# Kernel tuning notes

Hardware: AMD Instinct MI355X
Metric: run time of the kernel (lower is better)

Reference implementation:

```python
import jax, jax.numpy as jnp
import numpy as np

B, S, D_IN = 2, 2048, 1024
DIM, H, G = 64, 16, 4  # head dim, num_heads, kv groups


def setup_inputs() -> dict:
    key = jax.random.key(0)
    ks = jax.random.split(key, 9)
    query = jax.random.normal(ks[0], (B, S, D_IN), dtype=jnp.float32)
    key_t = jax.random.normal(ks[1], (B, S, D_IN), dtype=jnp.float32)
    value = jax.random.normal(ks[2], (B, S, D_IN), dtype=jnp.float32)
    # causal mask; masked_fill where mask == 0
    mask = jnp.tril(jnp.ones((S, S), dtype=jnp.int32))[None]  # [1,S,S]
    sc = 1.0 / np.sqrt(D_IN)
    Wq = jax.random.normal(ks[3], (H, D_IN, DIM), dtype=jnp.float32) * sc
    bq = jnp.zeros((H, DIM), dtype=jnp.float32)
    Wk = jax.random.normal(ks[4], (G, D_IN, DIM), dtype=jnp.float32) * sc
    bk = jnp.zeros((G, DIM), dtype=jnp.float32)
    Wv = jax.random.normal(ks[5], (G, D_IN, DIM), dtype=jnp.float32) * sc
    bv = jnp.zeros((G, DIM), dtype=jnp.float32)
    return {"query": query, "key": key_t, "value": value, "mask": mask,
            "Wq": Wq, "bq": bq, "Wk": Wk, "bk": bk, "Wv": Wv, "bv": bv}


def reference(query, key, value, mask, Wq, bq, Wk, bk, Wv, bv):
    # batched per-head projections (replaces the Python loop over heads)
    Q = jnp.einsum('bsd,hde->bhse', query, Wq) + bq[None, :, None, :]   # [B,H,S,E]
    K = jnp.einsum('bsd,gde->bgse', key, Wk) + bk[None, :, None, :]     # [B,G,S,E]
    V = jnp.einsum('bsd,gde->bgse', value, Wv) + bv[None, :, None, :]   # [B,G,S,E]
    # head i uses KV group i % G (as in the original loop)
    g_idx = jnp.arange(H) % G
    Kh = K[:, g_idx]  # [B,H,S,E]
    Vh = V[:, g_idx]
    attn = jnp.einsum('bhqe,bhke->bhqk', Q, Kh) / np.sqrt(DIM)          # [B,H,S,S]
    attn = jnp.where(mask[:, None] == 0, jnp.float32(-1e9), attn)
    p = jax.nn.softmax(attn, axis=-1)
    z = jnp.einsum('bhqk,bhke->bhqe', p, Vh)                             # [B,H,S,E]
    # concat heads along last dim (same order as torch.cat of z_list)
    return z.transpose(0, 2, 1, 3).reshape(B, S, H * DIM)
```

## Files before the change

kernel.cpp:

```cpp
#include <hip/hip_runtime.h>
#include <hip/hip_bf16.h>
#include <math.h>

#define S_LEN 2048
#define DIN   1024
#define NH    16
#define NG    4

typedef short s16x8 __attribute__((ext_vector_type(8)));
typedef float f32x4 __attribute__((ext_vector_type(4)));

__device__ __forceinline__ unsigned short f2bf(float x) {
  union { float f; unsigned u; } v; v.f = x;
  unsigned r = v.u + 0x7FFFu + ((v.u >> 16) & 1u);
  return (unsigned short)(r >> 16);
}
__device__ __forceinline__ unsigned cvtpk(float a, float b) {
  unsigned r;
  asm("v_cvt_pk_bf16_f32 %0, %1, %2" : "=v"(r) : "v"(a), "v"(b));
  return r;
}

#define GLOAD_LDS16(gsrc, ldst)                                              \
  __builtin_amdgcn_global_load_lds(                                         \
      (const __attribute__((address_space(1))) unsigned int*)(gsrc),        \
      (__attribute__((address_space(3))) unsigned int*)(ldst), 16, 0, 0)


__global__ __launch_bounds__(256) void k_cast(
    const float* __restrict__ q, const float* __restrict__ k,
    const float* __restrict__ v, unsigned short* __restrict__ AF) {
  const float* src = (blockIdx.y == 0) ? q : (blockIdx.y == 1) ? k : v;
  unsigned short* dst = AF + (size_t)blockIdx.y * 4194304;
  int flat = blockIdx.x * 256 + threadIdx.x;
  int b = flat >> 18, s = (flat >> 7) & 2047, d0 = (flat & 127) * 8;
  const float* sp = src + (size_t)(b * 2048 + s) * 1024 + d0;
  float4 x = *(const float4*)sp;
  float4 y = *(const float4*)(sp + 4);
  union { s16x8 v; unsigned u[4]; } r;
  r.u[0] = cvtpk(x.x, x.y); r.u[1] = cvtpk(x.z, x.w);
  r.u[2] = cvtpk(y.x, y.y); r.u[3] = cvtpk(y.z, y.w);
  unsigned short* p = dst + (size_t)((b * 128 + (s >> 4)) * 32 + (d0 >> 5)) * 512
                    + (s & 15) * 8 + ((d0 >> 3) & 3) * 128;
  *(s16x8*)p = r.v;
}

__global__ __launch_bounds__(256) void k_wtrans(
    const float* __restrict__ Wq, const float* __restrict__ Wk,
    const float* __restrict__ Wv, unsigned short* __restrict__ WF) {
  __shared__ __align__(16) unsigned short T[64][72];
  const int u = blockIdx.x >> 4, D0 = (blockIdx.x & 15) * 64;
  const int t = threadIdx.x;
  const float* src = (u < 16) ? (Wq + (size_t)u * 65536)
                   : (u < 20) ? (Wk + (size_t)(u - 16) * 65536)
                              : (Wv + (size_t)(u - 20) * 65536);
  const int e4 = (t & 15) * 4, dl = t >> 4;
  #pragma unroll
  for (int p = 0; p < 4; ++p) {
    const int d = p * 16 + dl;
    float4 v = *(const float4*)(src + (size_t)(D0 + d) * 64 + e4);
    T[e4 + 0][d] = f2bf(v.x); T[e4 + 1][d] = f2bf(v.y);
    T[e4 + 2][d] = f2bf(v.z); T[e4 + 3][d] = f2bf(v.w);
  }
  __syncthreads();
  const int j = t & 7;
  #pragma unroll
  for (int p = 0; p < 2; ++p) {
    const int e = p * 32 + (t >> 3);
    unsigned short* dst = WF + (size_t)u * 65536
        + (size_t)((e >> 4) * 32 + (D0 >> 5) + (j >> 2)) * 512
        + (e & 15) * 8 + (j & 3) * 128;
    *(s16x8*)dst = *(const s16x8*)&T[e][j * 8];
  }
}

__global__ __launch_bounds__(256, 4) void k_project(
    const unsigned short* __restrict__ AF,
    const float* __restrict__ bq, const float* __restrict__ bk,
    const float* __restrict__ bv,
    const unsigned short* __restrict__ WF,
    unsigned short* __restrict__ QF,
    unsigned short* __restrict__ KF,
    unsigned short* __restrict__ VF) {
  const int i = blockIdx.x;
  const int lid = (i & 7) * 96 + (i >> 3);
  const int strip = lid / 48;
  const int rr = lid % 48;
  const int b = rr / 24, u = rr % 24;
  const int tid = threadIdx.x;
  const int w = tid >> 6, lane = tid & 63, lq = lane & 15, gq = lane >> 4;

  const unsigned short* AFp = AF
      + (size_t)((u < 16) ? 0 : (u < 20) ? 1 : 2) * 4194304
      + (size_t)b * 2097152;
  const float* bias = (u < 16) ? bq + u * 64
                    : (u < 20) ? bk + (u - 16) * 64 : bv + (u - 20) * 64;
  const unsigned short* WFp = WF + (size_t)u * 65536;
  const int sb0 = strip * 8 + w * 2;
  const float OSC = (u < 16) ? 0.1803368801111204f : 1.0f;

  f32x4 acc[2][4] = {};
  s16x8 aE[2], bE[4], aO[2], bO[4];

  auto LD = [&](s16x8 (&a)[2], s16x8 (&bf)[4], int dk) {
    a[0] = *(const s16x8*)(AFp + (size_t)((sb0 + 0) * 32 + dk) * 512 + lane * 8);
    a[1] = *(const s16x8*)(AFp + (size_t)((sb0 + 1) * 32 + dk) * 512 + lane * 8);
    #pragma unroll
    for (int n = 0; n < 4; ++n)
      bf[n] = *(const s16x8*)(WFp + (size_t)(n * 32 + dk) * 512 + lane * 8);
  };
  auto FM = [&](const s16x8 (&a)[2], const s16x8 (&bf)[4]) {
    #pragma unroll
    for (int rf = 0; rf < 2; ++rf)
      #pragma unroll
      for (int n = 0; n < 4; ++n)
        acc[rf][n] = __builtin_amdgcn_mfma_f32_16x16x32_bf16(a[rf], bf[n], acc[rf][n], 0, 0, 0);
  };

  LD(aE, bE, 0);
  for (int dk = 0; dk < 32; dk += 2) {
    LD(aO, bO, dk + 1);
    FM(aE, bE);
    if (dk + 2 < 32) LD(aE, bE, dk + 2);
    FM(aO, bO);
  }

  float bvv[4];
  #pragma unroll
  for (int n = 0; n < 4; ++n) bvv[n] = bias[n * 16 + lq];

  unsigned short* dst = (u < 16) ? QF + (size_t)(b * 16 + u) * 131072
                      : (u < 20) ? KF + (size_t)(b * 4 + (u - 16)) * 131072
                                 : VF + (size_t)(b * 4 + (u - 20)) * 131072;
  #pragma unroll
  for (int rf = 0; rf < 2; ++rf)
    #pragma unroll
    for (int n = 0; n < 4; ++n)
      #pragma unroll
      for (int r = 0; r < 4; ++r) {
        const int s = strip * 128 + w * 32 + rf * 16 + gq * 4 + r;
        const int d = n * 16 + lq;
        const unsigned short hv = f2bf((acc[rf][n][r] + bvv[n]) * OSC);
        if (u < 20)
          dst[(size_t)((s >> 4) * 2 + (d >> 5)) * 512
              + (s & 15) * 8 + ((d >> 3) & 3) * 128 + (d & 7)] = hv;
        else
          dst[(size_t)(n * 64 + (s >> 5)) * 512
              + lq * 8 + ((s >> 3) & 3) * 128 + (s & 7)] = hv;
      }
}

__global__ __launch_bounds__(256) void k_attn(
    const unsigned short* __restrict__ QF, const unsigned short* __restrict__ KF,
    const unsigned short* __restrict__ VF, float* __restrict__ out) {
  __shared__ __align__(16) unsigned short KV[2][8192];
  __shared__ __align__(16) unsigned short P[4][16][72];
  const int tid = threadIdx.x;
  const int w = tid >> 6, lane = tid & 63, lq = lane & 15, gq = lane >> 4;
  const int x = blockIdx.x;
  const int xcd = x & 7, li = x >> 3;
  const int g = xcd & 3;
  const int j = 127 - (li * 2 + (xcd >> 2));
  const int h = g + 4 * w;
  const int b = blockIdx.y;

  const unsigned short* QFp = QF + (size_t)(b * NH + h) * 131072;
  const unsigned short* KFp = KF + (size_t)(b * NG + g) * 131072;
  const unsigned short* VFp = VF + (size_t)(b * NG + g) * 131072;
  const int nt = (j >> 2) + 1;

  const s16x8 qf0 = *(const s16x8*)(QFp + (size_t)(j * 2 + 0) * 512 + lane * 8);
  const s16x8 qf1 = *(const s16x8*)(QFp + (size_t)(j * 2 + 1) * 512 + lane * 8);
  f32x4 z[4] = {};
  float lsum = 0.f;

  auto stage = [&](int t, int buf) {
    const unsigned short* ks = KFp + (size_t)t * 4096 + (w * 2) * 512 + lane * 8;
    unsigned short* kd = &KV[buf][(w * 2) * 512];
    GLOAD_LDS16(ks, kd);
    GLOAD_LDS16(ks + 512, kd + 512);
    const unsigned short* vs = VFp + (size_t)(w * 64 + t * 2) * 512 + lane * 8;
    unsigned short* vd = &KV[buf][4096 + (w * 2) * 512];
    GLOAD_LDS16(vs, vd);
    GLOAD_LDS16(vs + 512, vd + 512);
  };

  auto tile = [&](int t, int buf) {
    const unsigned short* kb = &KV[buf][0];
    const unsigned short* vb = &KV[buf][4096];
    f32x4 sv[4];
    __builtin_amdgcn_s_setprio(1);
    #pragma unroll
    for (int f = 0; f < 4; ++f) {
      const s16x8 kA = *(const s16x8*)(kb + (f * 2 + 0) * 512 + lane * 8);
      const s16x8 kB = *(const s16x8*)(kb + (f * 2 + 1) * 512 + lane * 8);
      f32x4 s = {};
      s = __builtin_amdgcn_mfma_f32_16x16x32_bf16(kA, qf0, s, 0, 0, 0);
      s = __builtin_amdgcn_mfma_f32_16x16x32_bf16(kB, qf1, s, 0, 0, 0);
      sv[f] = s;
    }
    __builtin_amdgcn_s_setprio(0);
    if (t == nt - 1) {
      const int k0 = t * 64;
      const int qrow = j * 16 + lq;
      #pragma unroll
      for (int f = 0; f < 4; ++f)
        #pragma unroll
        for (int r = 0; r < 4; ++r)
          if (k0 + f * 16 + gq * 4 + r > qrow) sv[f][r] = -1e30f;
    }
    float s0 = 0.f, s1 = 0.f;
    #pragma unroll
    for (int f = 0; f < 4; ++f) {
      float p0 = __builtin_amdgcn_exp2f(sv[f][0]);
      float p1 = __builtin_amdgcn_exp2f(sv[f][1]);
      float p2 = __builtin_amdgcn_exp2f(sv[f][2]);
      float p3 = __builtin_amdgcn_exp2f(sv[f][3]);
      s0 += p0 + p1; s1 += p2 + p3;
      *(uint2*)&P[w][lq][f * 16 + gq * 4] = make_uint2(cvtpk(p0, p1), cvtpk(p2, p3));
    }
    lsum += s0 + s1;
    const s16x8 pa0 = *(const s16x8*)&P[w][lq][gq * 8];
    const s16x8 pa1 = *(const s16x8*)&P[w][lq][32 + gq * 8];
    __builtin_amdgcn_s_setprio(1);
    #pragma unroll
    for (int n = 0; n < 4; ++n) {
      const s16x8 v0 = *(const s16x8*)(vb + (n * 2 + 0) * 512 + lane * 8);
      const s16x8 v1 = *(const s16x8*)(vb + (n * 2 + 1) * 512 + lane * 8);
      z[n] = __builtin_amdgcn_mfma_f32_16x16x32_bf16(pa0, v0, z[n], 0, 0, 0);
      z[n] = __builtin_amdgcn_mfma_f32_16x16x32_bf16(pa1, v1, z[n], 0, 0, 0);
    }
    __builtin_amdgcn_s_setprio(0);
  };

  stage(0, 0);
  asm volatile("s_waitcnt vmcnt(0)");
  __syncthreads();
  int buf = 0;
  for (int t = 0; t < nt; ++t) {
    if (t + 1 < nt) stage(t + 1, buf ^ 1);
    tile(t, buf);
    asm volatile("s_waitcnt vmcnt(0)");
    __syncthreads();
    buf ^= 1;
  }

  lsum += __shfl_xor(lsum, 16);
  lsum += __shfl_xor(lsum, 32);
  float* outp = out + (size_t)b * S_LEN * 1024 + h * 64;
  #pragma unroll
  for (int r = 0; r < 4; ++r) {
    float lr = __shfl(lsum, gq * 4 + r, 64);
    float inv = __builtin_amdgcn_rcpf(lr);
    float* op = outp + (size_t)(j * 16 + gq * 4 + r) * 1024;
    #pragma unroll
    for (int n = 0; n < 4; ++n) op[n * 16 + lq] = z[n][r] * inv;
  }
}

extern "C" void kernel_launch(void* const* d_in, const int* in_sizes, int n_in,
                              void* d_out, int out_size, void* d_ws, size_t ws_size,
                              hipStream_t stream) {
  const float* query = (const float*)d_in[0];
  const float* key   = (const float*)d_in[1];
  const float* value = (const float*)d_in[2];
  const float* Wq = (const float*)d_in[4];
  const float* bq = (const float*)d_in[5];
  const float* Wk = (const float*)d_in[6];
  const float* bk = (const float*)d_in[7];
  const float* Wv = (const float*)d_in[8];
  const float* bv = (const float*)d_in[9];
  float* out = (float*)d_out;

  unsigned short* AF = (unsigned short*)d_ws;
  unsigned short* WF = AF + 12582912;
  unsigned short* QF = WF + 1572864;
  unsigned short* KF = QF + 4194304;
  unsigned short* VF = KF + 1048576;

  hipLaunchKernelGGL(k_cast, dim3(2048, 3), dim3(256), 0, stream,
                     query, key, value, AF);
  hipLaunchKernelGGL(k_wtrans, dim3(384), dim3(256), 0, stream, Wq, Wk, Wv, WF);
  hipLaunchKernelGGL(k_project, dim3(768), dim3(256), 0, stream,
                     AF, bq, bk, bv, WF, QF, KF, VF);
  hipLaunchKernelGGL(k_attn, dim3(512, 2), dim3(256), 0, stream, QF, KF, VF, out);
}
```

Baseline: 86.91 us.

## Stage cast through LDS for coalesced stores and halve projection tile height

The cast kernel now loads a 16x256 fp32 tile, converts it to bf16 into shared memory, then writes full contiguous 512-element fragment blocks. The aim is to replace the scattered 16-byte stores with coalesced ones. The projection kernel now gives each wave one 16-row fragment instead of two, doubles the grid and raises the occupancy hint to 6. This trades more parallelism against twice the weight-fragment reloads per output row.

```diff
diff --git a/kernel.cpp b/kernel.cpp
--- a/kernel.cpp
+++ b/kernel.cpp
@@ -30,19 +30,34 @@
 __global__ __launch_bounds__(256) void k_cast(
     const float* __restrict__ q, const float* __restrict__ k,
     const float* __restrict__ v, unsigned short* __restrict__ AF) {
-  const float* src = (blockIdx.y == 0) ? q : (blockIdx.y == 1) ? k : v;
-  unsigned short* dst = AF + (size_t)blockIdx.y * 4194304;
-  int flat = blockIdx.x * 256 + threadIdx.x;
-  int b = flat >> 18, s = (flat >> 7) & 2047, d0 = (flat & 127) * 8;
-  const float* sp = src + (size_t)(b * 2048 + s) * 1024 + d0;
-  float4 x = *(const float4*)sp;
-  float4 y = *(const float4*)(sp + 4);
-  union { s16x8 v; unsigned u[4]; } r;
-  r.u[0] = cvtpk(x.x, x.y); r.u[1] = cvtpk(x.z, x.w);
-  r.u[2] = cvtpk(y.x, y.y); r.u[3] = cvtpk(y.z, y.w);
-  unsigned short* p = dst + (size_t)((b * 128 + (s >> 4)) * 32 + (d0 >> 5)) * 512
-                    + (s & 15) * 8 + ((d0 >> 3) & 3) * 128;
-  *(s16x8*)p = r.v;
+  __shared__ __align__(16) unsigned short L[16][264];
+  const int i = blockIdx.y;
+  const float* src = (i == 0) ? q : (i == 1) ? k : v;
+  unsigned short* dst = AF + (size_t)i * 4194304;
+  const int x = blockIdx.x;
+  const int b = x >> 9, s16 = (x >> 2) & 127, dblk = x & 3;
+  const int t = threadIdx.x;
+  const float* base = src + ((size_t)(b * 2048 + s16 * 16)) * 1024 + dblk * 256;
+
+  #pragma unroll
+  for (int c = 0; c < 4; ++c) {
+    const int idx = c * 256 + t;
+    const int row = idx >> 6, c4 = (idx & 63) * 4;
+    float4 xv = *(const float4*)(base + (size_t)row * 1024 + c4);
+    *(uint2*)&L[row][c4] = make_uint2(cvtpk(xv.x, xv.y), cvtpk(xv.z, xv.w));
+  }
+  __syncthreads();
+
+  const int w = t >> 6, l = t & 63;
+  const int row = l & 15, kk = l >> 4;
+  #pragma unroll
+  for (int p = 0; p < 2; ++p) {
+    const int dk = w * 2 + p;
+    const s16x8 vreg = *(const s16x8*)&L[row][dk * 32 + kk * 8];
+    unsigned short* op = dst
+        + (size_t)((b * 128 + s16) * 32 + dblk * 8 + dk) * 512 + l * 8;
+    *(s16x8*)op = vreg;
+  }
 }
 
 __global__ __launch_bounds__(256) void k_wtrans(
@@ -74,7 +89,7 @@
   }
 }
 
-__global__ __launch_bounds__(256, 4) void k_project(
+__global__ __launch_bounds__(256, 6) void k_project(
     const unsigned short* __restrict__ AF,
     const float* __restrict__ bq, const float* __restrict__ bk,
     const float* __restrict__ bv,
@@ -83,7 +98,7 @@
     unsigned short* __restrict__ KF,
     unsigned short* __restrict__ VF) {
   const int i = blockIdx.x;
-  const int lid = (i & 7) * 96 + (i >> 3);
+  const int lid = (i & 7) * 192 + (i >> 3);
   const int strip = lid / 48;
   const int rr = lid % 48;
   const int b = rr / 24, u = rr % 24;
@@ -96,25 +111,22 @@
   const float* bias = (u < 16) ? bq + u * 64
                     : (u < 20) ? bk + (u - 16) * 64 : bv + (u - 20) * 64;
   const unsigned short* WFp = WF + (size_t)u * 65536;
-  const int sb0 = strip * 8 + w * 2;
+  const int sb0 = strip * 4 + w;
   const float OSC = (u < 16) ? 0.1803368801111204f : 1.0f;
 
-  f32x4 acc[2][4] = {};
-  s16x8 aE[2], bE[4], aO[2], bO[4];
-
-  auto LD = [&](s16x8 (&a)[2], s16x8 (&bf)[4], int dk) {
-    a[0] = *(const s16x8*)(AFp + (size_t)((sb0 + 0) * 32 + dk) * 512 + lane * 8);
-    a[1] = *(const s16x8*)(AFp + (size_t)((sb0 + 1) * 32 + dk) * 512 + lane * 8);
+  f32x4 acc[4] = {};
+  s16x8 aE, bE[4], aO, bO[4];
+
+  auto LD = [&](s16x8& a, s16x8 (&bf)[4], int dk) {
+    a = *(const s16x8*)(AFp + (size_t)(sb0 * 32 + dk) * 512 + lane * 8);
     #pragma unroll
     for (int n = 0; n < 4; ++n)
       bf[n] = *(const s16x8*)(WFp + (size_t)(n * 32 + dk) * 512 + lane * 8);
   };
-  auto FM = [&](const s16x8 (&a)[2], const s16x8 (&bf)[4]) {
-    #pragma unroll
-    for (int rf = 0; rf < 2; ++rf)
-      #pragma unroll
-      for (int n = 0; n < 4; ++n)
-        acc[rf][n] = __builtin_amdgcn_mfma_f32_16x16x32_bf16(a[rf], bf[n], acc[rf][n], 0, 0, 0);
+  auto FM = [&](const s16x8& a, const s16x8 (&bf)[4]) {
+    #pragma unroll
+    for (int n = 0; n < 4; ++n)
+      acc[n] = __builtin_amdgcn_mfma_f32_16x16x32_bf16(a, bf[n], acc[n], 0, 0, 0);
   };
 
   LD(aE, bE, 0);
@@ -133,21 +145,19 @@
                       : (u < 20) ? KF + (size_t)(b * 4 + (u - 16)) * 131072
                                  : VF + (size_t)(b * 4 + (u - 20)) * 131072;
   #pragma unroll
-  for (int rf = 0; rf < 2; ++rf)
-    #pragma unroll
-    for (int n = 0; n < 4; ++n)
-      #pragma unroll
-      for (int r = 0; r < 4; ++r) {
-        const int s = strip * 128 + w * 32 + rf * 16 + gq * 4 + r;
-        const int d = n * 16 + lq;
-        const unsigned short hv = f2bf((acc[rf][n][r] + bvv[n]) * OSC);
-        if (u < 20)
-          dst[(size_t)((s >> 4) * 2 + (d >> 5)) * 512
-              + (s & 15) * 8 + ((d >> 3) & 3) * 128 + (d & 7)] = hv;
-        else
-          dst[(size_t)(n * 64 + (s >> 5)) * 512
-              + lq * 8 + ((s >> 3) & 3) * 128 + (s & 7)] = hv;
-      }
+  for (int n = 0; n < 4; ++n)
+    #pragma unroll
+    for (int r = 0; r < 4; ++r) {
+      const int s = strip * 64 + w * 16 + gq * 4 + r;
+      const int d = n * 16 + lq;
+      const unsigned short hv = f2bf((acc[n][r] + bvv[n]) * OSC);
+      if (u < 20)
+        dst[(size_t)((s >> 4) * 2 + (d >> 5)) * 512
+            + (s & 15) * 8 + ((d >> 3) & 3) * 128 + (d & 7)] = hv;
+      else
+        dst[(size_t)(n * 64 + (s >> 5)) * 512
+            + lq * 8 + ((s >> 3) & 3) * 128 + (s & 7)] = hv;
+    }
 }
 
 __global__ __launch_bounds__(256) void k_attn(
@@ -278,10 +288,10 @@
   unsigned short* KF = QF + 4194304;
   unsigned short* VF = KF + 1048576;
 
-  hipLaunchKernelGGL(k_cast, dim3(2048, 3), dim3(256), 0, stream,
+  hipLaunchKernelGGL(k_cast, dim3(1024, 3), dim3(256), 0, stream,
                      query, key, value, AF);
   hipLaunchKernelGGL(k_wtrans, dim3(384), dim3(256), 0, stream, Wq, Wk, Wv, WF);
-  hipLaunchKernelGGL(k_project, dim3(768), dim3(256), 0, stream,
+  hipLaunchKernelGGL(k_project, dim3(1536), dim3(256), 0, stream,
                      AF, bq, bk, bv, WF, QF, KF, VF);
   hipLaunchKernelGGL(k_attn, dim3(512, 2), dim3(256), 0, stream, QF, KF, VF, out);
 }
```

Measured after the change: 92.34 us. 1.06x slower.
